# Optimization experiments

Measured on AMD Instinct MI355X. Metric: run time of the kernel, lower is better.

## Reference

```python
import jax, jax.numpy as jnp
import numpy as np

B, C, K, T = 8, 256, 64, 1000
NORM_EPS = 1e-12


def setup_inputs() -> dict:
    key = jax.random.key(0)
    k_x, k_codes, k_scales = jax.random.split(key, 3)
    init_val = 1.0 / (K * C) ** 0.5
    x = jax.random.normal(k_x, (B, C, T), dtype=jnp.float32)
    codes = jax.random.uniform(k_codes, (C, K), dtype=jnp.float32,
                               minval=-init_val, maxval=init_val)
    scales = jax.random.uniform(k_scales, (K,), dtype=jnp.float32,
                                minval=0.0, maxval=1.0)
    return {"x": x, "codes": codes, "scales": scales}


def l2_normalize(t, axis, eps=NORM_EPS):
    n = jnp.sqrt(jnp.sum(t * t, axis=axis, keepdims=True))
    n = jnp.maximum(n, eps)
    return t / n


def reference(x, codes, scales):
    # x: (B, C, T); codes: (C, K); scales: (K,)
    residual = x[:, :, None, :] - codes[None, :, :, None]      # (B, C, K, T)
    residual_l2sqr = jnp.sum(residual * residual, axis=1)      # (B, K, T)
    weights_tc = jax.nn.softmax(-scales[None, :, None] * residual_l2sqr, axis=1)  # softmax over codes K
    embeddings = jnp.einsum('bckt,bkt->bkc', residual, weights_tc) / x.shape[-1]  # (B, K, C)
    embeddings = l2_normalize(embeddings, axis=-1)
    return embeddings
```

## Files before the change

kernel.cpp:

```cpp
#include <hip/hip_runtime.h>
#include <stdint.h>

constexpr int Bn  = 8;
constexpr int Cn  = 256;
constexpr int Kn  = 64;
constexpr int Tn  = 1000;
constexpr int CH  = 16;
constexpr int NCH = 64;
constexpr int TW  = 256;
constexpr int NTQ = 4;

constexpr int XT_P = 264;
constexpr int MW_P = 20;
constexpr int XC_P = 264;

typedef float f32x4 __attribute__((ext_vector_type(4)));
typedef __bf16 bf16x8 __attribute__((ext_vector_type(8)));

__device__ __forceinline__ unsigned short f2bf(float f) {
    unsigned u = __float_as_uint(f);
    return (unsigned short)((u + 0x7FFFu + ((u >> 16) & 1u)) >> 16);
}

union BF8 { unsigned short u[8]; bf16x8 v; };

__global__ __launch_bounds__(256) void lde_w(
    const float* __restrict__ x,
    const float* __restrict__ codes,
    const float* __restrict__ scales,
    unsigned short* __restrict__ w_g,
    float* __restrict__ Sp)
{
    __shared__ __align__(16) unsigned short xT[CH * XT_P];
    __shared__ float Mw[Kn * MW_P];
    __shared__ float xsqp[64 * 17];
    __shared__ float xsq[CH];
    __shared__ float csqs[Kn];
    __shared__ float spw[4 * 64];

    const int tid  = threadIdx.x;
    const int wave = tid >> 6;
    const int lane = tid & 63;
    const int n    = lane & 15;
    const int q    = lane >> 4;
    const int b    = blockIdx.x >> 6;
    const int ch   = blockIdx.x & 63;
    const int t0   = ch * CH;
    const float* xb = x + (size_t)b * Cn * Tn;

    {
        const int tf = tid & 3;
        float sq0 = 0.f, sq1 = 0.f, sq2 = 0.f, sq3 = 0.f;
#pragma unroll
        for (int r = 0; r < 4; ++r) {
            int c = (tid >> 2) + 64 * r;
            int t = t0 + 4 * tf;
            float4 v;
            if (t + 3 < Tn) {
                v = *(const float4*)(xb + c * Tn + t);
            } else {
                v.x = (t     < Tn) ? xb[c * Tn + t]     : 0.f;
                v.y = (t + 1 < Tn) ? xb[c * Tn + t + 1] : 0.f;
                v.z = (t + 2 < Tn) ? xb[c * Tn + t + 2] : 0.f;
                v.w = (t + 3 < Tn) ? xb[c * Tn + t + 3] : 0.f;
            }
            xT[(4 * tf + 0) * XT_P + c] = f2bf(v.x);
            xT[(4 * tf + 1) * XT_P + c] = f2bf(v.y);
            xT[(4 * tf + 2) * XT_P + c] = f2bf(v.z);
            xT[(4 * tf + 3) * XT_P + c] = f2bf(v.w);
            sq0 = fmaf(v.x, v.x, sq0);
            sq1 = fmaf(v.y, v.y, sq1);
            sq2 = fmaf(v.z, v.z, sq2);
            sq3 = fmaf(v.w, v.w, sq3);
        }
        float* xp = xsqp + (tid >> 2) * 17 + 4 * tf;
        xp[0] = sq0; xp[1] = sq1; xp[2] = sq2; xp[3] = sq3;
    }
    __syncthreads();

    if (tid < CH) {
        float a = 0.f;
#pragma unroll
        for (int i = 0; i < 64; ++i) a += xsqp[i * 17 + tid];
        xsq[tid] = a;
    }

    {
        const int kglob = wave * 16 + n;
        const float* cod = codes + (q * 8) * Kn + kglob;
        float csq_part = 0.f;
        f32x4 acc = {0.f, 0.f, 0.f, 0.f};
#pragma unroll
        for (int c0 = 0; c0 < Cn; c0 += 32) {
            float cf[8];
#pragma unroll
            for (int j = 0; j < 8; ++j) cf[j] = cod[(size_t)(c0 + j) * Kn];
            BF8 aF;
#pragma unroll
            for (int j = 0; j < 8; ++j) {
                csq_part = fmaf(cf[j], cf[j], csq_part);
                aF.u[j] = f2bf(cf[j]);
            }
            bf16x8 bF = *(const bf16x8*)(xT + n * XT_P + c0 + q * 8);
            acc = __builtin_amdgcn_mfma_f32_16x16x32_bf16(aF.v, bF, acc, 0, 0, 0);
        }
        csq_part += __shfl_xor(csq_part, 16, 64);
        csq_part += __shfl_xor(csq_part, 32, 64);
        if (q == 0) csqs[kglob] = csq_part;
#pragma unroll
        for (int r = 0; r < 4; ++r)
            Mw[(wave * 16 + q * 4 + r) * MW_P + n] = acc[r];
    }
    __syncthreads();

    {
        const float sc = scales[lane];
        const float cq = csqs[lane];
        unsigned short wh[4];
        float sp = 0.f;
#pragma unroll
        for (int j = 0; j < 4; ++j) {
            int t = wave * 4 + j;
            float m     = Mw[lane * MW_P + t];
            float logit = -sc * (xsq[t] - 2.f * m + cq);
            float mx = logit;
#pragma unroll
            for (int off = 32; off >= 1; off >>= 1)
                mx = fmaxf(mx, __shfl_xor(mx, off, 64));
            float e = __expf(logit - mx);
            float s = e;
#pragma unroll
            for (int off = 32; off >= 1; off >>= 1)
                s += __shfl_xor(s, off, 64);
            float wv = e / s;
            if (t0 + t >= Tn) wv = 0.f;
            sp += wv;
            wh[j] = f2bf(wv);
        }
        *(ushort4*)(w_g + ((size_t)(b * NCH + ch) * Kn + lane) * CH + wave * 4) =
            make_ushort4(wh[0], wh[1], wh[2], wh[3]);
        spw[wave * 64 + lane] = sp;
    }
    __syncthreads();
    if (wave == 0) {
        float s4 = spw[lane] + spw[64 + lane] + spw[128 + lane] + spw[192 + lane];
        Sp[((size_t)b * Kn + lane) * NCH + ch] = s4;
    }
}

__global__ __launch_bounds__(256) void lde_pool(
    const float* __restrict__ x,
    const unsigned short* __restrict__ w_g,
    float* __restrict__ part)
{
    __shared__ __align__(16) unsigned short xc[16 * XC_P];

    const int tid  = threadIdx.x;
    const int wave = tid >> 6;
    const int lane = tid & 63;
    const int n    = lane & 15;
    const int q    = lane >> 4;
    const int bid  = blockIdx.x;
    const int b    = bid >> 6;
    const int ct   = (bid >> 2) & 15;
    const int tq   = bid & 3;
    const int c0   = ct * 16;
    const int tw0  = tq * TW;
    const float* xb = x + (size_t)(b * Cn + c0) * Tn;

#pragma unroll
    for (int r = 0; r < 4; ++r) {
        int idx = r * 256 + tid;
        int cl = idx >> 6, tf = idx & 63;
        int t = tw0 + 4 * tf;
        float4 v;
        if (t + 3 < Tn) {
            v = *(const float4*)(xb + cl * Tn + t);
        } else {
            v.x = (t     < Tn) ? xb[cl * Tn + t]     : 0.f;
            v.y = (t + 1 < Tn) ? xb[cl * Tn + t + 1] : 0.f;
            v.z = (t + 2 < Tn) ? xb[cl * Tn + t + 2] : 0.f;
            v.w = (t + 3 < Tn) ? xb[cl * Tn + t + 3] : 0.f;
        }
        *(ushort4*)(xc + cl * XC_P + 4 * tf) =
            make_ushort4(f2bf(v.x), f2bf(v.y), f2bf(v.z), f2bf(v.w));
    }
    __syncthreads();

    f32x4 acc = {0.f, 0.f, 0.f, 0.f};
#pragma unroll
    for (int s = 0; s < 8; ++s) {
        int tg  = tw0 + s * 32 + q * 8;
        int chh = tg >> 4;
        int tl  = tg & 15;
        bf16x8 aF = *(const bf16x8*)(w_g + ((size_t)(b * NCH + chh) * Kn + wave * 16 + n) * CH + tl);
        bf16x8 bF = *(const bf16x8*)(xc + n * XC_P + s * 32 + q * 8);
        acc = __builtin_amdgcn_mfma_f32_16x16x32_bf16(aF, bF, acc, 0, 0, 0);
    }
    float* pb = part + ((size_t)(b * NTQ + tq) * Kn + wave * 16 + q * 4) * Cn + c0 + n;
#pragma unroll
    for (int r = 0; r < 4; ++r)
        pb[(size_t)r * Cn] = acc[r];
}

__global__ __launch_bounds__(256) void lde_fin(
    const float* __restrict__ part,
    const float* __restrict__ Sp,
    const float* __restrict__ codes,
    float* __restrict__ out)
{
    const int b    = blockIdx.x >> 6;
    const int k    = blockIdx.x & 63;
    const int tid  = threadIdx.x;
    const int lane = tid & 63;
    const int wave = tid >> 6;

    __shared__ float red[4];
    __shared__ float Ss;

    if (wave == 0) {
        float s = Sp[((size_t)b * Kn + k) * NCH + lane];
#pragma unroll
        for (int off = 32; off >= 1; off >>= 1) s += __shfl_xor(s, off, 64);
        if (lane == 0) Ss = s;
    }
    __syncthreads();
    const float S = Ss;

    const int c = tid;
    const float* pb = part + (size_t)b * NTQ * Kn * Cn + k * Cn + c;
    float val = pb[0] + pb[(size_t)Kn * Cn] + pb[(size_t)2 * Kn * Cn] + pb[(size_t)3 * Kn * Cn];

    float e = (val - codes[c * Kn + k] * S) * (1.0f / (float)Tn);

    float qq = e * e;
#pragma unroll
    for (int off = 32; off >= 1; off >>= 1) qq += __shfl_xor(qq, off, 64);
    if (lane == 0) red[wave] = qq;
    __syncthreads();
    float nn = sqrtf(red[0] + red[1] + red[2] + red[3]);

    out[((size_t)b * Kn + k) * Cn + c] = e / fmaxf(nn, 1e-12f);
}

extern "C" void kernel_launch(void* const* d_in, const int* in_sizes, int n_in,
                              void* d_out, int out_size, void* d_ws, size_t ws_size,
                              hipStream_t stream) {
    const float* x      = (const float*)d_in[0];
    const float* codes  = (const float*)d_in[1];
    const float* scales = (const float*)d_in[2];
    float* out = (float*)d_out;

    char* ws = (char*)d_ws;
    float*          part = (float*)ws;
    unsigned short* w_g  = (unsigned short*)(ws + (2u << 20));
    float*          Sp   = (float*)(ws + (3u << 20));

    lde_w   <<<Bn * NCH,      256, 0, stream>>>(x, codes, scales, w_g, Sp);
    lde_pool<<<Bn * 16 * NTQ, 256, 0, stream>>>(x, w_g, part);
    lde_fin <<<Bn * Kn,       256, 0, stream>>>(part, Sp, codes, out);
}
```

Measured before the change: 75.73 us.

## Fuse finalize kernel into pool kernel via last-block atomic counter

Removes the separate finalize launch. Each pool block increments a per-batch atomic counter, and the last block for that batch reduces the partial sums, subtracts the codes term, L2-normalises and writes the output. The counter is reset in the first kernel. This saves one kernel launch and its gap, but the whole tail for each batch now runs on a single block with 4 waves, which serialises the 64 k rows.

```diff
diff --git a/kernel.cpp b/kernel.cpp
--- a/kernel.cpp
+++ b/kernel.cpp
@@ -29,7 +29,8 @@
     const float* __restrict__ codes,
     const float* __restrict__ scales,
     unsigned short* __restrict__ w_g,
-    float* __restrict__ Sp)
+    float* __restrict__ Sp,
+    int* __restrict__ cnt)
 {
     __shared__ __align__(16) unsigned short xT[CH * XT_P];
     __shared__ float Mw[Kn * MW_P];
@@ -47,6 +48,8 @@
     const int ch   = blockIdx.x & 63;
     const int t0   = ch * CH;
     const float* xb = x + (size_t)b * Cn * Tn;
+
+    if (ch == 0 && tid == 0) cnt[b] = 0;
 
     {
         const int tf = tid & 3;
@@ -151,9 +154,14 @@
 __global__ __launch_bounds__(256) void lde_pool(
     const float* __restrict__ x,
     const unsigned short* __restrict__ w_g,
-    float* __restrict__ part)
+    const float* __restrict__ Sp,
+    const float* __restrict__ codes,
+    float* __restrict__ part,
+    int* __restrict__ cnt,
+    float* __restrict__ out)
 {
     __shared__ __align__(16) unsigned short xc[16 * XC_P];
+    __shared__ int isLast;
 
     const int tid  = threadIdx.x;
     const int wave = tid >> 6;
@@ -201,46 +209,47 @@
 #pragma unroll
     for (int r = 0; r < 4; ++r)
         pb[(size_t)r * Cn] = acc[r];
-}
-
-__global__ __launch_bounds__(256) void lde_fin(
-    const float* __restrict__ part,
-    const float* __restrict__ Sp,
-    const float* __restrict__ codes,
-    float* __restrict__ out)
-{
-    const int b    = blockIdx.x >> 6;
-    const int k    = blockIdx.x & 63;
-    const int tid  = threadIdx.x;
-    const int lane = tid & 63;
-    const int wave = tid >> 6;
-
-    __shared__ float red[4];
-    __shared__ float Ss;
-
-    if (wave == 0) {
-        float s = Sp[((size_t)b * Kn + k) * NCH + lane];
-#pragma unroll
-        for (int off = 32; off >= 1; off >>= 1) s += __shfl_xor(s, off, 64);
-        if (lane == 0) Ss = s;
-    }
-    __syncthreads();
-    const float S = Ss;
-
-    const int c = tid;
-    const float* pb = part + (size_t)b * NTQ * Kn * Cn + k * Cn + c;
-    float val = pb[0] + pb[(size_t)Kn * Cn] + pb[(size_t)2 * Kn * Cn] + pb[(size_t)3 * Kn * Cn];
-
-    float e = (val - codes[c * Kn + k] * S) * (1.0f / (float)Tn);
-
-    float qq = e * e;
-#pragma unroll
-    for (int off = 32; off >= 1; off >>= 1) qq += __shfl_xor(qq, off, 64);
-    if (lane == 0) red[wave] = qq;
-    __syncthreads();
-    float nn = sqrtf(red[0] + red[1] + red[2] + red[3]);
-
-    out[((size_t)b * Kn + k) * Cn + c] = e / fmaxf(nn, 1e-12f);
+
+    if (tid == 0) {
+        __threadfence();
+        int old = __hip_atomic_fetch_add(&cnt[b], 1, __ATOMIC_ACQ_REL,
+                                         __HIP_MEMORY_SCOPE_AGENT);
+        isLast = (old == 63) ? 1 : 0;
+    }
+    __syncthreads();
+    if (!isLast) return;
+    __threadfence();
+
+    const float invT = 1.0f / (float)Tn;
+    const float* Spb  = Sp + (size_t)b * Kn * NCH;
+    const float* pbb  = part + (size_t)b * NTQ * Kn * Cn;
+    float* outb = out + (size_t)b * Kn * Cn;
+
+    for (int i = 0; i < 16; ++i) {
+        const int k = wave * 16 + i;
+        float S = Spb[(size_t)k * NCH + lane];
+#pragma unroll
+        for (int off = 32; off >= 1; off >>= 1) S += __shfl_xor(S, off, 64);
+
+        float e[4];
+        float qq = 0.f;
+#pragma unroll
+        for (int j = 0; j < 4; ++j) {
+            const int c = lane + 64 * j;
+            float val = 0.f;
+#pragma unroll
+            for (int t = 0; t < NTQ; ++t)
+                val += pbb[((size_t)t * Kn + k) * Cn + c];
+            e[j] = (val - codes[c * Kn + k] * S) * invT;
+            qq = fmaf(e[j], e[j], qq);
+        }
+#pragma unroll
+        for (int off = 32; off >= 1; off >>= 1) qq += __shfl_xor(qq, off, 64);
+        float rn = 1.0f / fmaxf(sqrtf(qq), 1e-12f);
+#pragma unroll
+        for (int j = 0; j < 4; ++j)
+            outb[(size_t)k * Cn + lane + 64 * j] = e[j] * rn;
+    }
 }
 
 extern "C" void kernel_launch(void* const* d_in, const int* in_sizes, int n_in,
@@ -255,8 +264,8 @@
     float*          part = (float*)ws;
     unsigned short* w_g  = (unsigned short*)(ws + (2u << 20));
     float*          Sp   = (float*)(ws + (3u << 20));
-
-    lde_w   <<<Bn * NCH,      256, 0, stream>>>(x, codes, scales, w_g, Sp);
-    lde_pool<<<Bn * 16 * NTQ, 256, 0, stream>>>(x, w_g, part);
-    lde_fin <<<Bn * Kn,       256, 0, stream>>>(part, Sp, codes, out);
-}
+    int*            cnt  = (int*)(ws + (3u << 20) + (128u << 10));
+
+    lde_w   <<<Bn * NCH,      256, 0, stream>>>(x, codes, scales, w_g, Sp, cnt);
+    lde_pool<<<Bn * 16 * NTQ, 256, 0, stream>>>(x, w_g, Sp, codes, part, cnt, out);
+}
```

After: 130.8 us. 1.73x slower.

## Replace split-T pooling kernel with single-wave full-T GEMM per K tile

Applied to the files above, without the earlier changes.

Replaces the pooling kernel, which staged x in shared memory and split T into four partial sums, with a one-wave-per-block kernel. Each block covers a 16-wide K tile and a 16-wide C tile, walks the full T range, and converts x to bf16 directly from global memory inside the MFMA loop. This removes the partial-sum buffer and the four-way reduction in the final kernel. The xsq reduction in the weight kernel is also parallelised across all four waves. In exchange, each x row is now reread by four blocks (one per K tile) without shared-memory reuse, and there is less parallelism within each block.

```diff
diff --git a/kernel.cpp b/kernel.cpp
--- a/kernel.cpp
+++ b/kernel.cpp
@@ -7,12 +7,9 @@
 constexpr int Tn  = 1000;
 constexpr int CH  = 16;
 constexpr int NCH = 64;
-constexpr int TW  = 256;
-constexpr int NTQ = 4;
 
 constexpr int XT_P = 264;
 constexpr int MW_P = 20;
-constexpr int XC_P = 264;
 
 typedef float f32x4 __attribute__((ext_vector_type(4)));
 typedef __bf16 bf16x8 __attribute__((ext_vector_type(8)));
@@ -34,7 +31,7 @@
     __shared__ __align__(16) unsigned short xT[CH * XT_P];
     __shared__ float Mw[Kn * MW_P];
     __shared__ float xsqp[64 * 17];
-    __shared__ float xsq[CH];
+    __shared__ float xsq4[64];
     __shared__ float csqs[Kn];
     __shared__ float spw[4 * 64];
 
@@ -78,11 +75,11 @@
     }
     __syncthreads();
 
-    if (tid < CH) {
+    if (lane < 16) {
         float a = 0.f;
 #pragma unroll
-        for (int i = 0; i < 64; ++i) a += xsqp[i * 17 + tid];
-        xsq[tid] = a;
+        for (int i = 0; i < 16; ++i) a += xsqp[(wave * 16 + i) * 17 + lane];
+        xsq4[wave * 16 + lane] = a;
     }
 
     {
@@ -121,8 +118,9 @@
 #pragma unroll
         for (int j = 0; j < 4; ++j) {
             int t = wave * 4 + j;
+            float xs_t  = xsq4[t] + xsq4[16 + t] + xsq4[32 + t] + xsq4[48 + t];
             float m     = Mw[lane * MW_P + t];
-            float logit = -sc * (xsq[t] - 2.f * m + cq);
+            float logit = -sc * (xs_t - 2.f * m + cq);
             float mx = logit;
 #pragma unroll
             for (int off = 32; off >= 1; off >>= 1)
@@ -148,63 +146,56 @@
     }
 }
 
-__global__ __launch_bounds__(256) void lde_pool(
+__global__ __launch_bounds__(64) void lde_gemm(
     const float* __restrict__ x,
     const unsigned short* __restrict__ w_g,
-    float* __restrict__ part)
+    float* __restrict__ Ew)
 {
-    __shared__ __align__(16) unsigned short xc[16 * XC_P];
-
-    const int tid  = threadIdx.x;
-    const int wave = tid >> 6;
-    const int lane = tid & 63;
+    const int lane = threadIdx.x;
     const int n    = lane & 15;
     const int q    = lane >> 4;
     const int bid  = blockIdx.x;
+    const int kt   = bid & 3;
+    const int ct   = (bid >> 2) & 15;
     const int b    = bid >> 6;
-    const int ct   = (bid >> 2) & 15;
-    const int tq   = bid & 3;
-    const int c0   = ct * 16;
-    const int tw0  = tq * TW;
-    const float* xb = x + (size_t)(b * Cn + c0) * Tn;
-
-#pragma unroll
-    for (int r = 0; r < 4; ++r) {
-        int idx = r * 256 + tid;
-        int cl = idx >> 6, tf = idx & 63;
-        int t = tw0 + 4 * tf;
-        float4 v;
-        if (t + 3 < Tn) {
-            v = *(const float4*)(xb + cl * Tn + t);
-        } else {
-            v.x = (t     < Tn) ? xb[cl * Tn + t]     : 0.f;
-            v.y = (t + 1 < Tn) ? xb[cl * Tn + t + 1] : 0.f;
-            v.z = (t + 2 < Tn) ? xb[cl * Tn + t + 2] : 0.f;
-            v.w = (t + 3 < Tn) ? xb[cl * Tn + t + 3] : 0.f;
-        }
-        *(ushort4*)(xc + cl * XC_P + 4 * tf) =
-            make_ushort4(f2bf(v.x), f2bf(v.y), f2bf(v.z), f2bf(v.w));
-    }
-    __syncthreads();
+
+    const float* xrow = x + (size_t)(b * Cn + ct * 16 + n) * Tn;
+    const unsigned short* wbase =
+        w_g + (size_t)b * NCH * Kn * CH + (kt * 16 + n) * CH + (q & 1) * 8;
+    const int qh = q >> 1;
 
     f32x4 acc = {0.f, 0.f, 0.f, 0.f};
-#pragma unroll
-    for (int s = 0; s < 8; ++s) {
-        int tg  = tw0 + s * 32 + q * 8;
-        int chh = tg >> 4;
-        int tl  = tg & 15;
-        bf16x8 aF = *(const bf16x8*)(w_g + ((size_t)(b * NCH + chh) * Kn + wave * 16 + n) * CH + tl);
-        bf16x8 bF = *(const bf16x8*)(xc + n * XC_P + s * 32 + q * 8);
-        acc = __builtin_amdgcn_mfma_f32_16x16x32_bf16(aF, bF, acc, 0, 0, 0);
-    }
-    float* pb = part + ((size_t)(b * NTQ + tq) * Kn + wave * 16 + q * 4) * Cn + c0 + n;
+#pragma unroll 4
+    for (int tc = 0; tc < 31; ++tc) {
+        bf16x8 aF = *(const bf16x8*)(wbase + (size_t)(2 * tc + qh) * (Kn * CH));
+        float4 v0 = *(const float4*)(xrow + tc * 32 + q * 8);
+        float4 v1 = *(const float4*)(xrow + tc * 32 + q * 8 + 4);
+        BF8 bF;
+        bF.u[0] = f2bf(v0.x); bF.u[1] = f2bf(v0.y);
+        bF.u[2] = f2bf(v0.z); bF.u[3] = f2bf(v0.w);
+        bF.u[4] = f2bf(v1.x); bF.u[5] = f2bf(v1.y);
+        bF.u[6] = f2bf(v1.z); bF.u[7] = f2bf(v1.w);
+        acc = __builtin_amdgcn_mfma_f32_16x16x32_bf16(aF, bF.v, acc, 0, 0, 0);
+    }
+    {
+        bf16x8 aF = *(const bf16x8*)(wbase + (size_t)(62 + qh) * (Kn * CH));
+        const int tbase = 31 * 32 + q * 8;
+        BF8 bF;
+#pragma unroll
+        for (int j = 0; j < 8; ++j) {
+            int t = tbase + j;
+            bF.u[j] = (t < Tn) ? f2bf(xrow[t]) : (unsigned short)0;
+        }
+        acc = __builtin_amdgcn_mfma_f32_16x16x32_bf16(aF, bF.v, acc, 0, 0, 0);
+    }
+    float* er = Ew + ((size_t)b * Kn + kt * 16 + q * 4) * Cn + ct * 16 + n;
 #pragma unroll
     for (int r = 0; r < 4; ++r)
-        pb[(size_t)r * Cn] = acc[r];
+        er[(size_t)r * Cn] = acc[r];
 }
 
 __global__ __launch_bounds__(256) void lde_fin(
-    const float* __restrict__ part,
+    const float* __restrict__ Ew,
     const float* __restrict__ Sp,
     const float* __restrict__ codes,
     float* __restrict__ out)
@@ -228,9 +219,7 @@
     const float S = Ss;
 
     const int c = tid;
-    const float* pb = part + (size_t)b * NTQ * Kn * Cn + k * Cn + c;
-    float val = pb[0] + pb[(size_t)Kn * Cn] + pb[(size_t)2 * Kn * Cn] + pb[(size_t)3 * Kn * Cn];
-
+    float val = Ew[((size_t)b * Kn + k) * Cn + c];
     float e = (val - codes[c * Kn + k] * S) * (1.0f / (float)Tn);
 
     float qq = e * e;
@@ -252,11 +241,11 @@
     float* out = (float*)d_out;
 
     char* ws = (char*)d_ws;
-    float*          part = (float*)ws;
-    unsigned short* w_g  = (unsigned short*)(ws + (2u << 20));
-    float*          Sp   = (float*)(ws + (3u << 20));
-
-    lde_w   <<<Bn * NCH,      256, 0, stream>>>(x, codes, scales, w_g, Sp);
-    lde_pool<<<Bn * 16 * NTQ, 256, 0, stream>>>(x, w_g, part);
-    lde_fin <<<Bn * Kn,       256, 0, stream>>>(part, Sp, codes, out);
-}
+    unsigned short* w_g = (unsigned short*)ws;
+    float*          Sp  = (float*)(ws + (1u << 20));
+    float*          Ew  = (float*)(ws + (1u << 20) + (128u << 10));
+
+    lde_w   <<<Bn * NCH,     256, 0, stream>>>(x, codes, scales, w_g, Sp);
+    lde_gemm<<<Bn * 16 * 4,  64,  0, stream>>>(x, w_g, Ew);
+    lde_fin <<<Bn * Kn,      256, 0, stream>>>(Ew, Sp, codes, out);
+}
```

Result: no change. 76.12 us (+0.5%).
